# Kernel optimization log

Hardware: AMD Instinct MI355X
Metric: run time of the kernel (lower is better)

## Reference

```python
import jax, jax.numpy as jnp
import numpy as np
import math

DEPTH = 3
RATIO = 0.5
EPS = 1e-5


def _mlp_ln(h, W1, b1, W2, b2, W3, b3, g, beta):
    h = jax.nn.gelu(h @ W1 + b1, approximate=False)
    h = jax.nn.gelu(h @ W2 + b2, approximate=False)
    h = h @ W3 + b3
    mu = jnp.mean(h, axis=-1, keepdims=True)
    var = jnp.mean((h - mu) ** 2, axis=-1, keepdims=True)
    return g * (h - mu) * jax.lax.rsqrt(var + EPS) + beta


def _node_to_node(x, s, r, n, p):
    # two-way gather -> scatter_add -> MLP+LN. Row n of x_pad is a zero dummy
    # node that absorbs edges dropped by pooling (fixed-size, jit-friendly).
    x_pad = jnp.concatenate([x, jnp.zeros((1, x.shape[1]), x.dtype)], axis=0)
    msg = x_pad[jnp.concatenate([s, r])]            # [2E, C]
    recv = jnp.concatenate([r, s])                  # [2E]
    agg = jax.ops.segment_sum(msg, recv, num_segments=n + 1)[:n]
    return _mlp_ln(agg, *p)


def _forward(x, senders, receivers, pool_w, down_p, up_p):
    s, r = senders, receivers
    xs, edges, perms = [x], [(s, r)], []
    n = x.shape[0]
    for i in range(DEPTH):
        k = math.ceil(RATIO * n)  # PyG topk: ceil(ratio * N)
        w = pool_w[i]
        score = jnp.tanh(x @ w / jnp.linalg.norm(w))
        vals, perm = jax.lax.top_k(score, k)
        x = x[perm] * vals[:, None]
        # remap edges; dropped nodes (and old dummy n) map to new dummy k
        nmap = jnp.full((n + 1,), k, dtype=s.dtype).at[perm].set(
            jnp.arange(k, dtype=s.dtype))
        ns_, nr_ = nmap[s], nmap[r]
        invalid = (ns_ == k) | (nr_ == k)
        s = jnp.where(invalid, k, ns_)
        r = jnp.where(invalid, k, nr_)
        x = _node_to_node(x, s, r, k, down_p[i])
        if i < DEPTH - 1:
            xs.append(x)
            edges.append((s, r))
        perms.append(perm)
        n = k
    for i in range(DEPTH):
        j = DEPTH - 1 - i
        res = xs[j]
        s, r = edges[j]
        perm = perms[j]
        up = jnp.zeros_like(res).at[perm].set(x)
        x = jnp.concatenate([res, up], axis=-1)  # sum_res=False -> concat
        x = _node_to_node(x, s, r, res.shape[0], up_p[i])
    return x


def setup_inputs() -> dict:
    key = jax.random.key(0)
    ks = jax.random.split(key, 16)
    N, E, C, D = 50000, 600000, 128, DEPTH
    f32 = jnp.float32

    def lin(k, fi, fo):
        return (jax.random.normal(k, (D, fi, fo), f32) / np.sqrt(fi)).astype(f32)

    return {
        'x': jax.random.normal(ks[0], (N, C), f32),
        'senders': jax.random.randint(ks[1], (E,), 0, N, dtype=jnp.int32),
        'receivers': jax.random.randint(ks[2], (E,), 0, N, dtype=jnp.int32),
        'pool_w': jax.random.normal(ks[3], (D, C), f32),
        'down_W1': lin(ks[4], C, C), 'down_b1': jnp.zeros((D, C), f32),
        'down_W2': lin(ks[5], C, C), 'down_b2': jnp.zeros((D, C), f32),
        'down_W3': lin(ks[6], C, C), 'down_b3': jnp.zeros((D, C), f32),
        'down_g': jnp.ones((D, C), f32), 'down_beta': jnp.zeros((D, C), f32),
        'up_W1': lin(ks[7], 2 * C, C), 'up_b1': jnp.zeros((D, C), f32),
        'up_W2': lin(ks[8], C, C), 'up_b2': jnp.zeros((D, C), f32),
        'up_W3': lin(ks[9], C, C), 'up_b3': jnp.zeros((D, C), f32),
        'up_g': jnp.ones((D, C), f32), 'up_beta': jnp.zeros((D, C), f32),
    }


def reference(x, senders, receivers, pool_w,
              down_W1, down_b1, down_W2, down_b2, down_W3, down_b3,
              down_g, down_beta,
              up_W1, up_b1, up_W2, up_b2, up_W3, up_b3, up_g, up_beta):
    down_p = [(down_W1[i], down_b1[i], down_W2[i], down_b2[i],
               down_W3[i], down_b3[i], down_g[i], down_beta[i])
              for i in range(DEPTH)]
    up_p = [(up_W1[i], up_b1[i], up_W2[i], up_b2[i],
             up_W3[i], up_b3[i], up_g[i], up_beta[i])
            for i in range(DEPTH)]
    return _forward(x, senders, receivers, pool_w, down_p, up_p)
```

## Files before the change

kernel.cpp:

```cpp
#include <hip/hip_runtime.h>
#include <math.h>


typedef unsigned short u16;
typedef short bf16x8 __attribute__((ext_vector_type(8)));
typedef float f32x4 __attribute__((ext_vector_type(4)));

#define HIST_STRIDE (2 * 65536 + 512)
#define NB 128
#define NB_LOG 7
#define SUBR 5000

__device__ __forceinline__ unsigned int fkey(float f) {
  unsigned int b = __float_as_uint(f);
  return (b & 0x80000000u) ? ~b : (b | 0x80000000u);
}

__device__ __forceinline__ float gelu_f(float v) {
  return 0.5f * v * (1.0f + erff(v * 0.70710678118654752f));
}

__device__ __forceinline__ u16 f2bf(float f) {
  unsigned u = __float_as_uint(f);
  u = (u + 0x7FFFu + ((u >> 16) & 1u)) >> 16;
  return (u16)u;
}
__device__ __forceinline__ float bf2f(u16 u) {
  return __uint_as_float(((unsigned)u) << 16);
}

__global__ void score_kernel(const float* __restrict__ x, const float* __restrict__ w,
                             float* __restrict__ key, float* __restrict__ valt, int n) {
  int wave = threadIdx.x >> 6, lane = threadIdx.x & 63;
  int i = blockIdx.x * 4 + wave;
  if (i >= n) return;
  float2 xv = *(const float2*)&x[(size_t)i * 128 + lane * 2];
  float2 wv = *(const float2*)&w[lane * 2];
  double d  = (double)xv.x * wv.x + (double)xv.y * wv.y;
  double nw = (double)wv.x * wv.x + (double)wv.y * wv.y;
  for (int o = 32; o; o >>= 1) { d += __shfl_down(d, o, 64); nw += __shfl_down(nw, o, 64); }
  if (lane == 0) {
    key[i]  = (float)d;
    valt[i] = (float)tanh(d / sqrt(nw));
  }
}

__global__ void preamble_kernel(const float* __restrict__ x, u16* __restrict__ xb, int n,
                                const float* __restrict__ uW1, const float* __restrict__ uW2,
                                const float* __restrict__ uW3, u16* __restrict__ wt1,
                                u16* __restrict__ wt2, u16* __restrict__ wt3,
                                const float* __restrict__ poolw, double* __restrict__ sqn,
                                u16* __restrict__ z0, u16* __restrict__ z1,
                                u16* __restrict__ z2, int* __restrict__ histAll,
                                int nbX, int nbHZ, int nHist) {
  int b = blockIdx.x;
  if (b < nbX) {
    int gid = b * 256 + threadIdx.x;
    if (gid < n * 32) {
      float4 a = *(const float4*)&x[(size_t)gid * 4];
      *(ushort4*)&xb[(size_t)gid * 4] =
          make_ushort4(f2bf(a.x), f2bf(a.y), f2bf(a.z), f2bf(a.w));
    }
    return;
  }
  b -= nbX;
  if (b < 768) {
    int i = b * 256 + threadIdx.x;
    int lvl = i >> 16, rem = i & 65535;
    if (rem < 32768) {
      int k = rem >> 7, c = rem & 127;
      wt1[(size_t)lvl * 32768 + c * 256 + k] = f2bf(uW1[(size_t)lvl * 32768 + rem]);
    } else if (rem < 49152) {
      int j = rem - 32768; int k = j >> 7, c = j & 127;
      wt2[(size_t)lvl * 16384 + c * 128 + k] = f2bf(uW2[(size_t)lvl * 16384 + j]);
    } else {
      int j = rem - 49152; int k = j >> 7, c = j & 127;
      wt3[(size_t)lvl * 16384 + c * 128 + k] = f2bf(uW3[(size_t)lvl * 16384 + j]);
    }
    return;
  }
  b -= 768;
  if (b == 0) {
    if (threadIdx.x < 64) {
      int lane = threadIdx.x;
      for (int l = 0; l < 3; ++l) {
        float2 wv = *(const float2*)&poolw[l * 128 + lane * 2];
        double nw = (double)wv.x * wv.x + (double)wv.y * wv.y;
        for (int o = 32; o; o >>= 1) nw += __shfl_down(nw, o, 64);
        if (lane == 0) sqn[l] = sqrt(nw);
      }
    }
    return;
  }
  b -= 1;
  if (b == 0) {
    int t = threadIdx.x;
    if (t < 128) { z0[t] = 0; z1[t] = 0; z2[t] = 0; }
    return;
  }
  b -= 1;
  {
    int i = b * 256 + threadIdx.x;
    if (i < nHist) histAll[i] = 0;
  }
}

__global__ void hist_hi_kernel(const float* __restrict__ key, int* __restrict__ hist,
                               int* __restrict__ csum, int n) {
  __shared__ int lc[256];
  lc[threadIdx.x] = 0;
  __syncthreads();
  int i = blockIdx.x * 256 + threadIdx.x;
  if (i < n) {
    unsigned b = fkey(key[i]) >> 16;
    atomicAdd(&hist[b], 1);
    atomicAdd(&lc[b >> 8], 1);
  }
  __syncthreads();
  int v = lc[threadIdx.x];
  if (v) atomicAdd(&csum[threadIdx.x], v);
}

__global__ void hist_lo_kernel(const float* __restrict__ key, const int* __restrict__ meta,
                               int* __restrict__ hist, int* __restrict__ csum, int n) {
  __shared__ int lc[256];
  lc[threadIdx.x] = 0;
  __syncthreads();
  int i = blockIdx.x * 256 + threadIdx.x;
  if (i < n) {
    unsigned u = fkey(key[i]);
    if ((u >> 16) == (unsigned)meta[0]) {
      unsigned b = u & 0xFFFFu;
      atomicAdd(&hist[b], 1);
      atomicAdd(&lc[b >> 8], 1);
    }
  }
  __syncthreads();
  int v = lc[threadIdx.x];
  if (v) atomicAdd(&csum[threadIdx.x], v);
}

__device__ __forceinline__ void suffix_scan256(int* sA, int t) {
  for (int o = 1; o < 256; o <<= 1) {
    int add = (t + o < 256) ? sA[t + o] : 0;
    __syncthreads();
    sA[t] += add;
    __syncthreads();
  }
}

__global__ void find_hi2_kernel(const int* __restrict__ hist, const int* __restrict__ csum,
                                int* __restrict__ meta, int k) {
  __shared__ int sA[256];
  __shared__ int cSh, cumSh;
  int t = threadIdx.x;
  sA[t] = csum[t];
  __syncthreads();
  suffix_scan256(sA, t);
  int nxt = (t == 255) ? 0 : sA[t + 1];
  if (sA[t] >= k && nxt < k) { cSh = t; cumSh = nxt; }
  __syncthreads();
  int c = cSh;
  int k2 = k - cumSh;
  sA[t] = hist[c * 256 + t];
  __syncthreads();
  suffix_scan256(sA, t);
  nxt = (t == 255) ? 0 : sA[t + 1];
  if (sA[t] >= k2 && nxt < k2) {
    meta[0] = c * 256 + t;
    meta[1] = k2 - nxt;
  }
}

__global__ void find_lo2_kernel(const int* __restrict__ hist, const int* __restrict__ csum,
                                int* __restrict__ meta) {
  __shared__ int sA[256];
  __shared__ int cSh, cumSh;
  int t = threadIdx.x;
  int m = meta[1], B = meta[0];
  sA[t] = csum[t];
  __syncthreads();
  suffix_scan256(sA, t);
  int nxt = (t == 255) ? 0 : sA[t + 1];
  if (sA[t] >= m && nxt < m) { cSh = t; cumSh = nxt; }
  __syncthreads();
  int c = cSh;
  int m2 = m - cumSh;
  sA[t] = hist[c * 256 + t];
  __syncthreads();
  suffix_scan256(sA, t);
  nxt = (t == 255) ? 0 : sA[t + 1];
  if (sA[t] >= m2 && nxt < m2) {
    meta[3] = (int)((((unsigned)B) << 16) | (unsigned)(c * 256 + t));
    meta[4] = m2 - nxt;
  }
  if (t == 0) meta[5] = 0;
}

__global__ void tie_count_kernel(const float* __restrict__ key, const int* __restrict__ meta,
                                 int* __restrict__ tcnt, int n) {
  __shared__ int cnt[4];
  unsigned uT = (unsigned)meta[3];
  int i = blockIdx.x * 256 + threadIdx.x;
  bool tie = (i < n) && (fkey(key[i]) == uT);
  unsigned long long m = __ballot(tie);
  int lane = threadIdx.x & 63, w = threadIdx.x >> 6;
  if (lane == 0) cnt[w] = __popcll(m);
  __syncthreads();
  if (threadIdx.x == 0) tcnt[blockIdx.x] = cnt[0] + cnt[1] + cnt[2] + cnt[3];
}

__global__ void tie_select_kernel(const float* __restrict__ key, const float* __restrict__ valt,
                                  const int* __restrict__ tcnt, int* __restrict__ meta,
                                  int* __restrict__ perm, float* __restrict__ vals,
                                  int* __restrict__ nmap, int n, int k) {
  __shared__ int red[256];
  __shared__ int woff[4];
  int t = threadIdx.x;
  red[t] = (t < (int)blockIdx.x) ? tcnt[t] : 0;
  __syncthreads();
  for (int s = 128; s; s >>= 1) {
    if (t < s) red[t] += red[t + s];
    __syncthreads();
  }
  int blockbase = red[0];
  unsigned uT = (unsigned)meta[3];
  int tsel = meta[4];
  int i = blockIdx.x * 256 + t;
  unsigned u = (i < n) ? fkey(key[i]) : 0u;
  bool tie = (i < n) && (u == uT);
  unsigned long long m = __ballot(tie);
  int lane = t & 63, w = t >> 6;
  if (lane == 0) woff[w] = __popcll(m);
  __syncthreads();
  if (t == 0) {
    int c = 0;
    for (int q = 0; q < 4; ++q) { int v = woff[q]; woff[q] = c; c += v; }
  }
  __syncthreads();
  if (i > n) return;
  if (i == n) { nmap[n] = k; return; }
  bool sel;
  if (tie) {
    int pre = __popcll(m & ((1ull << lane) - 1ull));
    int rank = blockbase + woff[w] + pre;
    sel = (rank < tsel);
  } else {
    sel = (u > uT);
  }
  if (sel) {
    int slot = atomicAdd(&meta[5], 1);
    perm[slot] = i; vals[slot] = valt[i]; nmap[i] = slot;
  } else {
    nmap[i] = k;
  }
}

__global__ void pool_kernel(const float* __restrict__ x, const int* __restrict__ perm,
                            const float* __restrict__ vals, float* __restrict__ xp, int k) {
  int gid = blockIdx.x * 256 + threadIdx.x;
  int t = gid >> 5;
  if (t >= k) return;
  int c = (gid & 31) << 2;
  float v = vals[t];
  float4 a = *(const float4*)&x[(size_t)perm[t] * 128 + c];
  a.x *= v; a.y *= v; a.z *= v; a.w *= v;
  *(float4*)&xp[(size_t)t * 128 + c] = a;
}

__global__ void csr_count_kernel(const int* __restrict__ s, const int* __restrict__ r,
                                 int* __restrict__ H, int N, int E, int CH) {
  __shared__ int cnt[SUBR];
  int b = blockIdx.x & (NB - 1);
  int sub = blockIdx.x >> NB_LOG;
  int base = sub * SUBR;
  int top = base + SUBR; if (top > N) top = N;
  int span = top - base;
  for (int t = threadIdx.x; t < span; t += 256) cnt[t] = 0;
  __syncthreads();
  int lo = b * CH, hi = lo + CH; if (hi > E) hi = E;
  for (int e = lo + threadIdx.x; e < hi; e += 256) {
    int sv = s[e], rv = r[e];
    if ((unsigned)(rv - base) < (unsigned)span) atomicAdd(&cnt[rv - base], 1);
    if ((unsigned)(sv - base) < (unsigned)span) atomicAdd(&cnt[sv - base], 1);
  }
  __syncthreads();
  int* Hb = H + (size_t)b * N + base;
  for (int t = threadIdx.x; t < span; t += 256) Hb[t] = cnt[t];
}

__global__ void colsum_part_kernel(const int* __restrict__ H, int* __restrict__ deg,
                                   int* __restrict__ bsum, int n) {
  __shared__ int l[256];
  int i = blockIdx.x * 256 + threadIdx.x;
  int v = 0;
  if (i < n) {
#pragma unroll 4
    for (int b = 0; b < NB; ++b) v += H[(size_t)b * n + i];
    deg[i] = v;
  }
  l[threadIdx.x] = (i < n) ? v : 0;
  __syncthreads();
  for (int s = 128; s; s >>= 1) {
    if (threadIdx.x < s) l[threadIdx.x] += l[threadIdx.x + s];
    __syncthreads();
  }
  if (threadIdx.x == 0) bsum[blockIdx.x] = l[0];
}

__global__ void scanfix_kernel(const int* __restrict__ deg, const int* __restrict__ bsum,
                               int* __restrict__ off, int* __restrict__ H, int n) {
  __shared__ int red[256];
  __shared__ int l[256];
  int i = blockIdx.x * 256 + threadIdx.x;
  int t = threadIdx.x;
  red[t] = (t < (int)blockIdx.x) ? bsum[t] : 0;
  __syncthreads();
  for (int s = 128; s; s >>= 1) {
    if (t < s) red[t] += red[t + s];
    __syncthreads();
  }
  int base = red[0];
  int v = (i < n) ? deg[i] : 0;
  l[t] = v;
  __syncthreads();
#pragma unroll
  for (int s = 1; s < 256; s <<= 1) {
    int add = (t >= s) ? l[t - s] : 0;
    __syncthreads();
    l[t] += add;
    __syncthreads();
  }
  int incl = l[t];
  if (i < n) {
    int e = base + incl - v;
    off[i] = e;
    if (i == n - 1) off[n] = base + incl;
    int run = e;
#pragma unroll 4
    for (int b = 0; b < NB; ++b) {
      size_t id = (size_t)b * n + i;
      int tv = H[id];
      H[id] = run;
      run += tv;
    }
  }
}

__global__ void csr_scatter_lds_kernel(const int* __restrict__ s, const int* __restrict__ r,
                                       const int* __restrict__ H, int* __restrict__ idx,
                                       int N, int E, int CH) {
  __shared__ int cnt[SUBR];
  int b = blockIdx.x & (NB - 1);
  int sub = blockIdx.x >> NB_LOG;
  int base = sub * SUBR;
  int top = base + SUBR; if (top > N) top = N;
  int span = top - base;
  for (int t = threadIdx.x; t < span; t += 256) cnt[t] = 0;
  __syncthreads();
  int lo = b * CH, hi = lo + CH; if (hi > E) hi = E;
  const int* Hb = H + (size_t)b * N;
  for (int e = lo + threadIdx.x; e < hi; e += 256) {
    int sv = s[e], rv = r[e];
    if ((unsigned)(rv - base) < (unsigned)span) {
      int loc = atomicAdd(&cnt[rv - base], 1);
      idx[Hb[rv] + loc] = sv;
    }
    if ((unsigned)(sv - base) < (unsigned)span) {
      int loc = atomicAdd(&cnt[sv - base], 1);
      idx[Hb[sv] + loc] = rv;
    }
  }
}

__global__ void derive_deg_kernel(const int* __restrict__ permL, const int* __restrict__ nm,
                                  const int* __restrict__ offP, const int* __restrict__ idxP,
                                  int* __restrict__ deg, int k) {
  int wave = threadIdx.x >> 6, lane = threadIdx.x & 63;
  int v = blockIdx.x * 4 + wave;
  if (v >= k) return;
  int p = permL[v];
  int lo = __builtin_amdgcn_readfirstlane(offP[p]);
  int hi = __builtin_amdgcn_readfirstlane(offP[p + 1]);
  int cnt = 0;
  for (int j0 = lo; j0 < hi; j0 += 64) {
    int j = j0 + lane;
    bool ok = (j < hi) && (nm[idxP[j]] < k);
    unsigned long long msk = __ballot(ok);
    cnt += __popcll(msk);
  }
  if (lane == 0) deg[v] = cnt;
}

__global__ void derive_fill_kernel(const int* __restrict__ permL, const int* __restrict__ nm,
                                   const int* __restrict__ offP, const int* __restrict__ idxP,
                                   const int* __restrict__ offL, int* __restrict__ idxL,
                                   int k) {
  int wave = threadIdx.x >> 6, lane = threadIdx.x & 63;
  int v = blockIdx.x * 4 + wave;
  if (v >= k) return;
  int p = permL[v];
  int lo = __builtin_amdgcn_readfirstlane(offP[p]);
  int hi = __builtin_amdgcn_readfirstlane(offP[p + 1]);
  int base = __builtin_amdgcn_readfirstlane(offL[v]);
  for (int j0 = lo; j0 < hi; j0 += 64) {
    int j = j0 + lane;
    int m = k;
    if (j < hi) m = nm[idxP[j]];
    bool ok = m < k;
    unsigned long long msk = __ballot(ok);
    int rank = __popcll(msk & ((1ull << lane) - 1ull));
    if (ok) idxL[base + rank] = m;
    base += __popcll(msk);
  }
}

__global__ void scan_part_kernel(const int* __restrict__ deg, int* __restrict__ bsum, int n) {
  __shared__ int l[256];
  int i = blockIdx.x * 256 + threadIdx.x;
  l[threadIdx.x] = (i < n) ? deg[i] : 0;
  __syncthreads();
  for (int s = 128; s; s >>= 1) {
    if (threadIdx.x < s) l[threadIdx.x] += l[threadIdx.x + s];
    __syncthreads();
  }
  if (threadIdx.x == 0) bsum[blockIdx.x] = l[0];
}

__global__ void scan_final_kernel(const int* __restrict__ deg, const int* __restrict__ bsum,
                                  int* __restrict__ off, int n) {
  __shared__ int red[256];
  __shared__ int l[256];
  int i = blockIdx.x * 256 + threadIdx.x;
  int t = threadIdx.x;
  red[t] = (t < (int)blockIdx.x) ? bsum[t] : 0;
  __syncthreads();
  for (int s = 128; s; s >>= 1) {
    if (t < s) red[t] += red[t + s];
    __syncthreads();
  }
  int base = red[0];
  int v = (i < n) ? deg[i] : 0;
  l[t] = v;
  __syncthreads();
#pragma unroll
  for (int s = 1; s < 256; s <<= 1) {
    int add = (t >= s) ? l[t - s] : 0;
    __syncthreads();
    l[t] += add;
    __syncthreads();
  }
  int incl = l[t];
  if (i < n) {
    int e = base + incl - v;
    off[i] = e;
    if (i == n - 1) off[n] = base + incl;
  }
}

__global__ void idxup3_kernel(const int* __restrict__ idxA, const int* __restrict__ nmA,
                              const int* __restrict__ lenA, int* __restrict__ outA,
                              const int* __restrict__ idxB, const int* __restrict__ nmB,
                              const int* __restrict__ lenB, int* __restrict__ outB,
                              const int* __restrict__ idxC, const int* __restrict__ nmC,
                              const int* __restrict__ lenC, int* __restrict__ outC,
                              int nbSeg, int maxlen) {
  int seg = blockIdx.x / nbSeg;
  int j = (blockIdx.x - seg * nbSeg) * 256 + threadIdx.x;
  if (j >= maxlen) return;
  const int* idx; const int* nm; const int* len; int* out;
  if (seg == 0)      { idx = idxA; nm = nmA; len = lenA; out = outA; }
  else if (seg == 1) { idx = idxB; nm = nmB; len = lenB; out = outB; }
  else               { idx = idxC; nm = nmC; len = lenC; out = outC; }
  if (j >= len[0]) return;
  out[j] = nm[idx[j]];
}

__global__ void agg_kernel(const float* __restrict__ x, const int* __restrict__ off,
                           const int* __restrict__ idx, float* __restrict__ agg, int n) {
  int wave = threadIdx.x >> 6, lane = threadIdx.x & 63;
  int v = blockIdx.x * 4 + wave;
  if (v >= n) return;
  int lo = __builtin_amdgcn_readfirstlane(off[v]);
  int hi = __builtin_amdgcn_readfirstlane(off[v + 1]);
  int g = lane >> 5, sl = lane & 31;
  const float* bp = x + sl * 4;
  float4 acc = {0.f, 0.f, 0.f, 0.f};
#define ACC_F(EE)                                        \
  do {                                                   \
    float4 w_ = *(const float4*)(bp + (size_t)(EE) * 128);\
    acc.x += w_.x; acc.y += w_.y; acc.z += w_.z; acc.w += w_.w; \
  } while (0)
  int j = lo;
  for (; j + 8 <= hi; j += 8) {
    int q0 = idx[j],     q1 = idx[j + 1], q2 = idx[j + 2], q3 = idx[j + 3];
    int q4 = idx[j + 4], q5 = idx[j + 5], q6 = idx[j + 6], q7 = idx[j + 7];
    ACC_F(g ? q1 : q0);
    ACC_F(g ? q3 : q2);
    ACC_F(g ? q5 : q4);
    ACC_F(g ? q7 : q6);
  }
  for (; j + 2 <= hi; j += 2) {
    int q0 = idx[j], q1 = idx[j + 1];
    ACC_F(g ? q1 : q0);
  }
  if (j < hi) {
    int q0 = idx[j];
    if (!g) ACC_F(q0);
  }
#undef ACC_F
  acc.x += __shfl_xor(acc.x, 32, 64);
  acc.y += __shfl_xor(acc.y, 32, 64);
  acc.z += __shfl_xor(acc.z, 32, 64);
  acc.w += __shfl_xor(acc.w, 32, 64);
  if (!g) *(float4*)&agg[(size_t)v * 128 + sl * 4] = acc;
}

__global__ void agg_gather2_kernel(const u16* __restrict__ tabR, const int* __restrict__ idxR,
                                   const u16* __restrict__ tabU, const int* __restrict__ idxU,
                                   const int* __restrict__ off, u16* __restrict__ agg,
                                   int n, int nbHalf) {
  bool upH = (int)blockIdx.x >= nbHalf;
  int blk = upH ? (int)blockIdx.x - nbHalf : (int)blockIdx.x;
  const u16* tab = upH ? tabU : tabR;
  const int* idx = upH ? idxU : idxR;
  int OFS = upH ? 128 : 0;
  int wave = threadIdx.x >> 6, lane = threadIdx.x & 63;
  int v = blk * 4 + wave;
  if (v >= n) return;
  int lo = __builtin_amdgcn_readfirstlane(off[v]);
  int hi = __builtin_amdgcn_readfirstlane(off[v + 1]);
  int g = lane >> 4, sl = lane & 15;
  const u16* bp = tab + sl * 8;
  float4 a0 = {0.f, 0.f, 0.f, 0.f}, a1 = {0.f, 0.f, 0.f, 0.f};

#define ACC_ROW(EE)                                     \
  do {                                                  \
    uint4 wq = *(const uint4*)(bp + (size_t)(EE) * 128);\
    a0.x += __uint_as_float(wq.x << 16);                \
    a0.y += __uint_as_float(wq.x & 0xffff0000u);        \
    a0.z += __uint_as_float(wq.y << 16);                \
    a0.w += __uint_as_float(wq.y & 0xffff0000u);        \
    a1.x += __uint_as_float(wq.z << 16);                \
    a1.y += __uint_as_float(wq.z & 0xffff0000u);        \
    a1.z += __uint_as_float(wq.w << 16);                \
    a1.w += __uint_as_float(wq.w & 0xffff0000u);        \
  } while (0)

  int j = lo;
  for (; j + 16 <= hi; j += 16) {
    int e0 = idx[j + g];
    int e1 = idx[j + g + 4];
    int e2 = idx[j + g + 8];
    int e3 = idx[j + g + 12];
    ACC_ROW(e0); ACC_ROW(e1); ACC_ROW(e2); ACC_ROW(e3);
  }
  for (; j + 4 <= hi; j += 4) {
    int e0 = idx[j + g];
    ACC_ROW(e0);
  }
  int rmn = hi - j;
  if (g < rmn) {
    int e = idx[j + g];
    ACC_ROW(e);
  }
#undef ACC_ROW

  a0.x += __shfl_xor(a0.x, 16, 64);
  a0.y += __shfl_xor(a0.y, 16, 64);
  a0.z += __shfl_xor(a0.z, 16, 64);
  a0.w += __shfl_xor(a0.w, 16, 64);
  a1.x += __shfl_xor(a1.x, 16, 64);
  a1.y += __shfl_xor(a1.y, 16, 64);
  a1.z += __shfl_xor(a1.z, 16, 64);
  a1.w += __shfl_xor(a1.w, 16, 64);
  a0.x += __shfl_xor(a0.x, 32, 64);
  a0.y += __shfl_xor(a0.y, 32, 64);
  a0.z += __shfl_xor(a0.z, 32, 64);
  a0.w += __shfl_xor(a0.w, 32, 64);
  a1.x += __shfl_xor(a1.x, 32, 64);
  a1.y += __shfl_xor(a1.y, 32, 64);
  a1.z += __shfl_xor(a1.z, 32, 64);
  a1.w += __shfl_xor(a1.w, 32, 64);

  if (lane < 16) {
    bf16x8 ov;
    ov[0] = (short)f2bf(a0.x); ov[1] = (short)f2bf(a0.y);
    ov[2] = (short)f2bf(a0.z); ov[3] = (short)f2bf(a0.w);
    ov[4] = (short)f2bf(a1.x); ov[5] = (short)f2bf(a1.y);
    ov[6] = (short)f2bf(a1.z); ov[7] = (short)f2bf(a1.w);
    *(bf16x8*)&agg[(size_t)v * 256 + OFS + sl * 8] = ov;
  }
}

template <bool SCORE>
__global__ __launch_bounds__(256) void mlp_down_kernel(
    const float* __restrict__ A,
    const float* __restrict__ W1, const float* __restrict__ b1,
    const float* __restrict__ W2, const float* __restrict__ b2,
    const float* __restrict__ W3, const float* __restrict__ b3,
    const float* __restrict__ g, const float* __restrict__ beta,
    float* __restrict__ out, u16* __restrict__ outbf,
    const float* __restrict__ wnext, const double* __restrict__ sqn,
    float* __restrict__ key, float* __restrict__ valt, int n) {
  __shared__ float cur[32 * 128];
  __shared__ float As[32 * 32];
  __shared__ float Ws[32 * 128];
  int t = threadIdx.x;
  int row0 = blockIdx.x * 32;
  int colg = (t & 31) << 2;
  int rowg = (t >> 5) << 2;
  float acc[4][4];
  const float* Wl[3] = {W1, W2, W3};
  const float* bl[3] = {b1, b2, b3};
#pragma unroll
  for (int l = 0; l < 3; ++l) {
    const float* W = Wl[l];
#pragma unroll
    for (int i = 0; i < 4; ++i)
#pragma unroll
      for (int j = 0; j < 4; ++j) acc[i][j] = 0.f;
    for (int k0 = 0; k0 < 128; k0 += 32) {
      __syncthreads();
      {
        int ar = t >> 3, ac = (t & 7) << 2;
        float4 av;
        if (l == 0) {
          av = make_float4(0.f, 0.f, 0.f, 0.f);
          if (row0 + ar < n) av = *(const float4*)&A[(size_t)(row0 + ar) * 128 + k0 + ac];
        } else {
          av = *(const float4*)&cur[ar * 128 + k0 + ac];
        }
        *(float4*)&As[ar * 32 + ac] = av;
      }
#pragma unroll
      for (int ll = 0; ll < 4; ++ll) {
        int id = t + ll * 256;
        int kk = id >> 5, wc = (id & 31) << 2;
        *(float4*)&Ws[kk * 128 + wc] = *(const float4*)&W[(size_t)(k0 + kk) * 128 + wc];
      }
      __syncthreads();
#pragma unroll
      for (int kk = 0; kk < 32; kk += 4) {
        float4 wv[4];
#pragma unroll
        for (int j = 0; j < 4; ++j) wv[j] = *(const float4*)&Ws[(kk + j) * 128 + colg];
#pragma unroll
        for (int i = 0; i < 4; ++i) {
          float4 av = *(const float4*)&As[(rowg + i) * 32 + kk];
          acc[i][0] += av.x * wv[0].x + av.y * wv[1].x + av.z * wv[2].x + av.w * wv[3].x;
          acc[i][1] += av.x * wv[0].y + av.y * wv[1].y + av.z * wv[2].y + av.w * wv[3].y;
          acc[i][2] += av.x * wv[0].z + av.y * wv[1].z + av.z * wv[2].z + av.w * wv[3].z;
          acc[i][3] += av.x * wv[0].w + av.y * wv[1].w + av.z * wv[2].w + av.w * wv[3].w;
        }
      }
    }
    float4 bv = *(const float4*)&bl[l][colg];
    if (l < 2) {
      __syncthreads();
#pragma unroll
      for (int i = 0; i < 4; ++i) {
        float4 o = make_float4(gelu_f(acc[i][0] + bv.x), gelu_f(acc[i][1] + bv.y),
                               gelu_f(acc[i][2] + bv.z), gelu_f(acc[i][3] + bv.w));
        *(float4*)&cur[(rowg + i) * 128 + colg] = o;
      }
    } else {
#pragma unroll
      for (int i = 0; i < 4; ++i) {
        acc[i][0] += bv.x; acc[i][1] += bv.y; acc[i][2] += bv.z; acc[i][3] += bv.w;
      }
    }
  }
  float4 gvv = *(const float4*)&g[colg];
  float4 bev = *(const float4*)&beta[colg];
  float4 wv4 = make_float4(0.f, 0.f, 0.f, 0.f);
  if (SCORE) wv4 = *(const float4*)&wnext[colg];
#pragma unroll
  for (int i = 0; i < 4; ++i) {
    float s1 = acc[i][0] + acc[i][1] + acc[i][2] + acc[i][3];
#pragma unroll
    for (int o = 1; o <= 16; o <<= 1) s1 += __shfl_xor(s1, o, 64);
    float mu = s1 * (1.0f / 128.0f);
    float d0 = acc[i][0] - mu, d1 = acc[i][1] - mu, d2 = acc[i][2] - mu, d3 = acc[i][3] - mu;
    float s2 = d0 * d0 + d1 * d1 + d2 * d2 + d3 * d3;
#pragma unroll
    for (int o = 1; o <= 16; o <<= 1) s2 += __shfl_xor(s2, o, 64);
    float rs = rsqrtf(s2 * (1.0f / 128.0f) + 1e-5f);
    int rr = row0 + rowg + i;
    float o0 = gvv.x * d0 * rs + bev.x;
    float o1 = gvv.y * d1 * rs + bev.y;
    float o2 = gvv.z * d2 * rs + bev.z;
    float o3 = gvv.w * d3 * rs + bev.w;
    if (rr < n) {
      *(float4*)&out[(size_t)rr * 128 + colg] = make_float4(o0, o1, o2, o3);
      *(ushort4*)&outbf[(size_t)rr * 128 + colg] =
          make_ushort4(f2bf(o0), f2bf(o1), f2bf(o2), f2bf(o3));
    }
    if (SCORE) {
      double d = (double)o0 * wv4.x + (double)o1 * wv4.y +
                 (double)o2 * wv4.z + (double)o3 * wv4.w;
#pragma unroll
      for (int o = 1; o <= 16; o <<= 1) d += __shfl_xor(d, o, 64);
      if ((t & 31) == 0 && rr < n) {
        key[rr]  = (float)d;
        valt[rr] = (float)tanh(d / sqn[0]);
      }
    }
  }
}

template <bool WF32, bool WBF>
__global__ __launch_bounds__(256) void mlp_up_kernel(
    const u16* __restrict__ A,
    const u16* __restrict__ WT1, const float* __restrict__ b1,
    const u16* __restrict__ WT2, const float* __restrict__ b2,
    const u16* __restrict__ WT3, const float* __restrict__ b3,
    const float* __restrict__ g, const float* __restrict__ beta,
    float* __restrict__ out, u16* __restrict__ outbf, int n) {
  __shared__ u16 As[64 * 72];
  __shared__ u16 Ws[128 * 72];
  __shared__ u16 cur[64 * 136];
  int t = threadIdx.x;
  int lane = t & 63, wave = t >> 6;
  int row0 = blockIdx.x * 64;
  int colb = lane & 15, rquad = lane >> 4;
  f32x4 acc[8];

#pragma unroll
  for (int i = 0; i < 8; ++i) acc[i] = (f32x4){0.f, 0.f, 0.f, 0.f};
  for (int k0 = 0; k0 < 256; k0 += 64) {
    __syncthreads();
#pragma unroll
    for (int i = 0; i < 2; ++i) {
      int c = t + i * 256;
      int r = c >> 3, seg = c & 7;
      bf16x8 v = {0, 0, 0, 0, 0, 0, 0, 0};
      if (row0 + r < n) v = *(const bf16x8*)&A[(size_t)(row0 + r) * 256 + k0 + seg * 8];
      *(bf16x8*)&As[r * 72 + seg * 8] = v;
    }
#pragma unroll
    for (int i = 0; i < 4; ++i) {
      int c = t + i * 256;
      int r = c >> 3, seg = c & 7;
      *(bf16x8*)&Ws[r * 72 + seg * 8] = *(const bf16x8*)&WT1[(size_t)r * 256 + k0 + seg * 8];
    }
    __syncthreads();
#pragma unroll
    for (int kk = 0; kk < 64; kk += 32) {
      bf16x8 a = *(const bf16x8*)&As[(wave * 16 + (lane & 15)) * 72 + kk + (lane >> 4) * 8];
#pragma unroll
      for (int ct = 0; ct < 8; ++ct) {
        bf16x8 b = *(const bf16x8*)&Ws[(ct * 16 + (lane & 15)) * 72 + kk + (lane >> 4) * 8];
        acc[ct] = __builtin_amdgcn_mfma_f32_16x16x32_bf16(a, b, acc[ct], 0, 0, 0);
      }
    }
  }
  __syncthreads();
#pragma unroll
  for (int ct = 0; ct < 8; ++ct) {
    int col = ct * 16 + colb;
    float bb = b1[col];
#pragma unroll
    for (int r = 0; r < 4; ++r) {
      int row = wave * 16 + rquad * 4 + r;
      cur[row * 136 + col] = f2bf(gelu_f(acc[ct][r] + bb));
    }
  }

#pragma unroll
  for (int i = 0; i < 8; ++i) acc[i] = (f32x4){0.f, 0.f, 0.f, 0.f};
  for (int k0 = 0; k0 < 128; k0 += 64) {
    __syncthreads();
#pragma unroll
    for (int i = 0; i < 4; ++i) {
      int c = t + i * 256;
      int r = c >> 3, seg = c & 7;
      *(bf16x8*)&Ws[r * 72 + seg * 8] = *(const bf16x8*)&WT2[(size_t)r * 128 + k0 + seg * 8];
    }
    __syncthreads();
#pragma unroll
    for (int kk = 0; kk < 64; kk += 32) {
      bf16x8 a = *(const bf16x8*)&cur[(wave * 16 + (lane & 15)) * 136 + k0 + kk + (lane >> 4) * 8];
#pragma unroll
      for (int ct = 0; ct < 8; ++ct) {
        bf16x8 b = *(const bf16x8*)&Ws[(ct * 16 + (lane & 15)) * 72 + kk + (lane >> 4) * 8];
        acc[ct] = __builtin_amdgcn_mfma_f32_16x16x32_bf16(a, b, acc[ct], 0, 0, 0);
      }
    }
  }
  __syncthreads();
#pragma unroll
  for (int ct = 0; ct < 8; ++ct) {
    int col = ct * 16 + colb;
    float bb = b2[col];
#pragma unroll
    for (int r = 0; r < 4; ++r) {
      int row = wave * 16 + rquad * 4 + r;
      cur[row * 136 + col] = f2bf(gelu_f(acc[ct][r] + bb));
    }
  }

#pragma unroll
  for (int i = 0; i < 8; ++i) acc[i] = (f32x4){0.f, 0.f, 0.f, 0.f};
  for (int k0 = 0; k0 < 128; k0 += 64) {
    __syncthreads();
#pragma unroll
    for (int i = 0; i < 4; ++i) {
      int c = t + i * 256;
      int r = c >> 3, seg = c & 7;
      *(bf16x8*)&Ws[r * 72 + seg * 8] = *(const bf16x8*)&WT3[(size_t)r * 128 + k0 + seg * 8];
    }
    __syncthreads();
#pragma unroll
    for (int kk = 0; kk < 64; kk += 32) {
      bf16x8 a = *(const bf16x8*)&cur[(wave * 16 + (lane & 15)) * 136 + k0 + kk + (lane >> 4) * 8];
#pragma unroll
      for (int ct = 0; ct < 8; ++ct) {
        bf16x8 b = *(const bf16x8*)&Ws[(ct * 16 + (lane & 15)) * 72 + kk + (lane >> 4) * 8];
        acc[ct] = __builtin_amdgcn_mfma_f32_16x16x32_bf16(a, b, acc[ct], 0, 0, 0);
      }
    }
  }
  float bv[8], gv[8], bev[8];
#pragma unroll
  for (int ct = 0; ct < 8; ++ct) {
    int col = ct * 16 + colb;
    bv[ct] = b3[col]; gv[ct] = g[col]; bev[ct] = beta[col];
  }
#pragma unroll
  for (int r = 0; r < 4; ++r) {
    float s1 = 0.f;
#pragma unroll
    for (int ct = 0; ct < 8; ++ct) s1 += acc[ct][r] + bv[ct];
#pragma unroll
    for (int o = 1; o <= 8; o <<= 1) s1 += __shfl_xor(s1, o, 64);
    float mu = s1 * (1.0f / 128.0f);
    float s2 = 0.f;
#pragma unroll
    for (int ct = 0; ct < 8; ++ct) { float d = acc[ct][r] + bv[ct] - mu; s2 += d * d; }
#pragma unroll
    for (int o = 1; o <= 8; o <<= 1) s2 += __shfl_xor(s2, o, 64);
    float rs = rsqrtf(s2 * (1.0f / 128.0f) + 1e-5f);
    int row = row0 + wave * 16 + rquad * 4 + r;
    if (row < n) {
#pragma unroll
      for (int ct = 0; ct < 8; ++ct) {
        int col = ct * 16 + colb;
        float o = gv[ct] * (acc[ct][r] + bv[ct] - mu) * rs + bev[ct];
        if (WF32) out[(size_t)row * 128 + col] = o;
        if (WBF)  outbf[(size_t)row * 128 + col] = f2bf(o);
      }
    }
  }
}


static inline int cdiv(int a, int b) { return (a + b - 1) / b; }

extern "C" void kernel_launch(void* const* d_in, const int* in_sizes, int n_in,
                              void* d_out, int out_size, void* d_ws, size_t ws_size,
                              hipStream_t stream) {
  const float* x0   = (const float*)d_in[0];
  const int*   snd  = (const int*)d_in[1];
  const int*   rcv  = (const int*)d_in[2];
  const float* poolw = (const float*)d_in[3];
  const float* dW1 = (const float*)d_in[4];
  const float* db1 = (const float*)d_in[5];
  const float* dW2 = (const float*)d_in[6];
  const float* db2 = (const float*)d_in[7];
  const float* dW3 = (const float*)d_in[8];
  const float* db3 = (const float*)d_in[9];
  const float* dg  = (const float*)d_in[10];
  const float* dbe = (const float*)d_in[11];
  const float* uW1 = (const float*)d_in[12];
  const float* ub1 = (const float*)d_in[13];
  const float* uW2 = (const float*)d_in[14];
  const float* ub2 = (const float*)d_in[15];
  const float* uW3 = (const float*)d_in[16];
  const float* ub3 = (const float*)d_in[17];
  const float* ug  = (const float*)d_in[18];
  const float* ube = (const float*)d_in[19];

  const int N0 = in_sizes[0] / 128;
  const int E  = in_sizes[1];
  const int N1 = (N0 + 1) / 2, N2 = (N1 + 1) / 2, N3 = (N2 + 1) / 2;

  char* p = (char*)d_ws;
  auto alloc = [&](size_t bytes) -> void* {
    void* r = (void*)p;
    p += (bytes + 255) & ~(size_t)255;
    return r;
  };
  float* key  = (float*)alloc((size_t)N0 * 4);
  float* valt = (float*)alloc((size_t)N0 * 4);
  int*   histAll = (int*)alloc((size_t)3 * HIST_STRIDE * 4);
  int*   meta = (int*)alloc(64 * 4);
  int*   tcnt = (int*)alloc(512 * 4);
  int*   bsum = (int*)alloc(256 * 4);
  int*   nm1 = (int*)alloc((size_t)(N0 + 1) * 4);
  int*   nm2 = (int*)alloc((size_t)(N1 + 1) * 4);
  int*   nm3 = (int*)alloc((size_t)(N2 + 1) * 4);
  int*   perm0 = (int*)alloc((size_t)N1 * 4);
  int*   perm1 = (int*)alloc((size_t)N2 * 4);
  int*   perm2 = (int*)alloc((size_t)N3 * 4);
  float* vals  = (float*)alloc((size_t)N1 * 4);
  double* sqn  = (double*)alloc(8 * 8);
  float* x1 = (float*)alloc((size_t)N1 * 128 * 4);
  float* x2 = (float*)alloc((size_t)N2 * 128 * 4);
  float* x3 = (float*)alloc((size_t)N3 * 128 * 4);
  float* xp = (float*)alloc((size_t)N1 * 128 * 4);
  float* aggf = (float*)alloc((size_t)N1 * 128 * 4);
  u16* agg_bf = (u16*)alloc((size_t)N0 * 256 * 2);
  u16* res0_bf = (u16*)alloc((size_t)N0 * 128 * 2);
  u16* res1_bf = (u16*)alloc((size_t)N1 * 128 * 2);
  u16* res2_bf = (u16*)alloc((size_t)N2 * 128 * 2);
  u16* x3_bf   = (u16*)alloc((size_t)(N3 + 1) * 128 * 2);
  u16* xu2_bf  = (u16*)alloc((size_t)(N2 + 1) * 128 * 2);
  u16* xu1_bf  = (u16*)alloc((size_t)(N1 + 1) * 128 * 2);
  u16* wt1 = (u16*)alloc((size_t)3 * 128 * 256 * 2);
  u16* wt2 = (u16*)alloc((size_t)3 * 128 * 128 * 2);
  u16* wt3 = (u16*)alloc((size_t)3 * 128 * 128 * 2);
  int* degAll = (int*)alloc((size_t)(N0 + N1 + N2 + N3) * 4);
  int* deg0 = degAll;
  int* deg1 = degAll + N0;
  int* deg2 = deg1 + N1;
  int* deg3 = deg2 + N2;
  int* off0 = (int*)alloc((size_t)(N0 + 1) * 4);
  int* idx0 = (int*)alloc((size_t)2 * E * 4);
  int* off1 = (int*)alloc((size_t)(N1 + 1) * 4);
  int* idx1 = (int*)alloc((size_t)2 * E * 4);
  int* off2 = (int*)alloc((size_t)(N2 + 1) * 4);
  int* idx2 = (int*)alloc((size_t)2 * E * 4);
  int* off3 = (int*)alloc((size_t)(N3 + 1) * 4);
  int* idx3 = (int*)alloc((size_t)2 * E * 4);
  int* idxu0 = (int*)alloc((size_t)2 * E * 4);
  int* idxu1 = (int*)alloc((size_t)2 * E * 4);
  int* idxu2 = (int*)alloc((size_t)2 * E * 4);
  int* H = (int*)alloc((size_t)NB * N0 * 4);

  {
    int nbX = cdiv(N0 * 32, 256);
    int nHist = 3 * HIST_STRIDE;
    int nbHZ = cdiv(nHist, 256);
    preamble_kernel<<<nbX + 768 + 1 + 1 + nbHZ, 256, 0, stream>>>(
        x0, res0_bf, N0, uW1, uW2, uW3, wt1, wt2, wt3, poolw, sqn,
        x3_bf + (size_t)N3 * 128, xu2_bf + (size_t)N2 * 128,
        xu1_bf + (size_t)N1 * 128, histAll, nbX, nbHZ, nHist);
  }

  {
    int nSub = cdiv(N0, SUBR);
    int CH = cdiv(E, NB);
    int nbN = cdiv(N0, 256);
    csr_count_kernel<<<NB * nSub, 256, 0, stream>>>(snd, rcv, H, N0, E, CH);
    colsum_part_kernel<<<nbN, 256, 0, stream>>>(H, deg0, bsum, N0);
    scanfix_kernel<<<nbN, 256, 0, stream>>>(deg0, bsum, off0, H, N0);
    csr_scatter_lds_kernel<<<NB * nSub, 256, 0, stream>>>(snd, rcv, H, idx0, N0, E, CH);
  }

  auto run_scan = [&](int* degB, int* offB, int n) {
    int nb = cdiv(n, 256);
    scan_part_kernel<<<nb, 256, 0, stream>>>(degB, bsum, n);
    scan_final_kernel<<<nb, 256, 0, stream>>>(degB, bsum, offB, n);
  };

  auto down_step = [&](int n, int k, const float* xcur, int* permL, int* nmL,
                       float* xnext, u16* xnext_bf, int lvl,
                       const int* offP, const int* idxP,
                       int* offL, int* degL, int* idxL) {
    int nb = cdiv(n, 256);
    int* histL = histAll + (size_t)lvl * HIST_STRIDE;
    int* csum_hi = histL + 2 * 65536;
    int* csum_lo = csum_hi + 256;
    hist_hi_kernel<<<nb, 256, 0, stream>>>(key, histL, csum_hi, n);
    find_hi2_kernel<<<1, 256, 0, stream>>>(histL, csum_hi, meta, k);
    hist_lo_kernel<<<nb, 256, 0, stream>>>(key, meta, histL + 65536, csum_lo, n);
    find_lo2_kernel<<<1, 256, 0, stream>>>(histL + 65536, csum_lo, meta);
    tie_count_kernel<<<nb, 256, 0, stream>>>(key, meta, tcnt, n);
    tie_select_kernel<<<cdiv(n + 1, 256), 256, 0, stream>>>(
        key, valt, tcnt, meta, permL, vals, nmL, n, k);
    pool_kernel<<<cdiv(k * 32, 256), 256, 0, stream>>>(xcur, permL, vals, xp, k);
    derive_deg_kernel<<<cdiv(k, 4), 256, 0, stream>>>(permL, nmL, offP, idxP, degL, k);
    run_scan(degL, offL, k);
    derive_fill_kernel<<<cdiv(k, 4), 256, 0, stream>>>(permL, nmL, offP, idxP, offL, idxL, k);
    agg_kernel<<<cdiv(k, 4), 256, 0, stream>>>(xp, offL, idxL, aggf, k);
    if (lvl < 2)
      mlp_down_kernel<true><<<cdiv(k, 32), 256, 0, stream>>>(
          aggf,
          dW1 + (size_t)lvl * 128 * 128, db1 + (size_t)lvl * 128,
          dW2 + (size_t)lvl * 128 * 128, db2 + (size_t)lvl * 128,
          dW3 + (size_t)lvl * 128 * 128, db3 + (size_t)lvl * 128,
          dg + (size_t)lvl * 128, dbe + (size_t)lvl * 128,
          xnext, xnext_bf, poolw + (size_t)(lvl + 1) * 128, sqn + (lvl + 1),
          key, valt, k);
    else
      mlp_down_kernel<false><<<cdiv(k, 32), 256, 0, stream>>>(
          aggf,
          dW1 + (size_t)lvl * 128 * 128, db1 + (size_t)lvl * 128,
          dW2 + (size_t)lvl * 128 * 128, db2 + (size_t)lvl * 128,
          dW3 + (size_t)lvl * 128 * 128, db3 + (size_t)lvl * 128,
          dg + (size_t)lvl * 128, dbe + (size_t)lvl * 128,
          xnext, xnext_bf, nullptr, nullptr, nullptr, nullptr, k);
  };

  score_kernel<<<cdiv(N0, 4), 256, 0, stream>>>(x0, poolw, key, valt, N0);
  down_step(N0, N1, x0, perm0, nm1, x1, res1_bf, 0, off0, idx0, off1, deg1, idx1);
  down_step(N1, N2, x1, perm1, nm2, x2, res2_bf, 1, off1, idx1, off2, deg2, idx2);
  down_step(N2, N3, x2, perm2, nm3, x3, x3_bf,   2, off2, idx2, off3, deg3, idx3);

  {
    int nbSeg = cdiv(2 * E, 256);
    idxup3_kernel<<<3 * nbSeg, 256, 0, stream>>>(
        idx2, nm3, off2 + N2, idxu2,
        idx1, nm2, off1 + N1, idxu1,
        idx0, nm1, off0 + N0, idxu0, nbSeg, 2 * E);
  }

  auto up_step = [&](int n, const u16* resb, const u16* xdb, int lvl,
                     const int* offL, const int* idxL, const int* idxUL,
                     bool wantF32, float* outF32, u16* outBF) {
    int nbh = cdiv(n, 4);
    agg_gather2_kernel<<<2 * nbh, 256, 0, stream>>>(
        resb, idxL, xdb, idxUL, offL, agg_bf, n, nbh);
    if (wantF32)
      mlp_up_kernel<true, false><<<cdiv(n, 64), 256, 0, stream>>>(
          agg_bf,
          wt1 + (size_t)lvl * 128 * 256, ub1 + (size_t)lvl * 128,
          wt2 + (size_t)lvl * 128 * 128, ub2 + (size_t)lvl * 128,
          wt3 + (size_t)lvl * 128 * 128, ub3 + (size_t)lvl * 128,
          ug + (size_t)lvl * 128, ube + (size_t)lvl * 128,
          outF32, nullptr, n);
    else
      mlp_up_kernel<false, true><<<cdiv(n, 64), 256, 0, stream>>>(
          agg_bf,
          wt1 + (size_t)lvl * 128 * 256, ub1 + (size_t)lvl * 128,
          wt2 + (size_t)lvl * 128 * 128, ub2 + (size_t)lvl * 128,
          wt3 + (size_t)lvl * 128 * 128, ub3 + (size_t)lvl * 128,
          ug + (size_t)lvl * 128, ube + (size_t)lvl * 128,
          nullptr, outBF, n);
  };

  up_step(N2, res2_bf, x3_bf,  0, off2, idx2, idxu2, false, nullptr, xu2_bf);
  up_step(N1, res1_bf, xu2_bf, 1, off1, idx1, idxu1, false, nullptr, xu1_bf);
  up_step(N0, res0_bf, xu1_bf, 2, off0, idx0, idxu0, true, (float*)d_out, nullptr);

  (void)n_in; (void)out_size; (void)ws_size;
}
```

Measured before the change: 821.1 us.

## Merge pool and degree kernels, single-block scan, split down MLP into three GEMMs

Pooling and degree counting now run as one launch, with blocks dispatched by index range. The two-kernel block scan is replaced by a single-block serial scan over all k entries. The fused three-layer down MLP kernel is split into two GEMM+GELU kernels and a GEMM+LayerNorm kernel, which write intermediates to new global buffers. This removes launch overhead and LDS pressure per kernel, but adds global round trips for the intermediates and serialises the scan onto one block.

```diff
diff --git a/kernel.cpp b/kernel.cpp
--- a/kernel.cpp
+++ b/kernel.cpp
@@ -256,16 +256,38 @@
   }
 }
 
-__global__ void pool_kernel(const float* __restrict__ x, const int* __restrict__ perm,
-                            const float* __restrict__ vals, float* __restrict__ xp, int k) {
-  int gid = blockIdx.x * 256 + threadIdx.x;
-  int t = gid >> 5;
-  if (t >= k) return;
-  int c = (gid & 31) << 2;
-  float v = vals[t];
-  float4 a = *(const float4*)&x[(size_t)perm[t] * 128 + c];
-  a.x *= v; a.y *= v; a.z *= v; a.w *= v;
-  *(float4*)&xp[(size_t)t * 128 + c] = a;
+__global__ void pool_derive_kernel(const float* __restrict__ x, const int* __restrict__ perm,
+                                   const float* __restrict__ vals, float* __restrict__ xp,
+                                   const int* __restrict__ nm, const int* __restrict__ offP,
+                                   const int* __restrict__ idxP, int* __restrict__ deg,
+                                   int k, int nbPool) {
+  int b = blockIdx.x;
+  if (b < nbPool) {
+    int gid = b * 256 + threadIdx.x;
+    int tt = gid >> 5;
+    if (tt >= k) return;
+    int c = (gid & 31) << 2;
+    float v = vals[tt];
+    float4 a = *(const float4*)&x[(size_t)perm[tt] * 128 + c];
+    a.x *= v; a.y *= v; a.z *= v; a.w *= v;
+    *(float4*)&xp[(size_t)tt * 128 + c] = a;
+    return;
+  }
+  b -= nbPool;
+  int wave = threadIdx.x >> 6, lane = threadIdx.x & 63;
+  int v = b * 4 + wave;
+  if (v >= k) return;
+  int p = perm[v];
+  int lo = __builtin_amdgcn_readfirstlane(offP[p]);
+  int hi = __builtin_amdgcn_readfirstlane(offP[p + 1]);
+  int cnt = 0;
+  for (int j0 = lo; j0 < hi; j0 += 64) {
+    int j = j0 + lane;
+    bool ok = (j < hi) && (nm[idxP[j]] < k);
+    unsigned long long msk = __ballot(ok);
+    cnt += __popcll(msk);
+  }
+  if (lane == 0) deg[v] = cnt;
 }
 
 __global__ void csr_count_kernel(const int* __restrict__ s, const int* __restrict__ r,
@@ -371,25 +393,6 @@
       idx[Hb[sv] + loc] = rv;
     }
   }
-}
-
-__global__ void derive_deg_kernel(const int* __restrict__ permL, const int* __restrict__ nm,
-                                  const int* __restrict__ offP, const int* __restrict__ idxP,
-                                  int* __restrict__ deg, int k) {
-  int wave = threadIdx.x >> 6, lane = threadIdx.x & 63;
-  int v = blockIdx.x * 4 + wave;
-  if (v >= k) return;
-  int p = permL[v];
-  int lo = __builtin_amdgcn_readfirstlane(offP[p]);
-  int hi = __builtin_amdgcn_readfirstlane(offP[p + 1]);
-  int cnt = 0;
-  for (int j0 = lo; j0 < hi; j0 += 64) {
-    int j = j0 + lane;
-    bool ok = (j < hi) && (nm[idxP[j]] < k);
-    unsigned long long msk = __ballot(ok);
-    cnt += __popcll(msk);
-  }
-  if (lane == 0) deg[v] = cnt;
 }
 
 __global__ void derive_fill_kernel(const int* __restrict__ permL, const int* __restrict__ nm,
@@ -415,46 +418,31 @@
   }
 }
 
-__global__ void scan_part_kernel(const int* __restrict__ deg, int* __restrict__ bsum, int n) {
+__global__ void scan_single_kernel(const int* __restrict__ deg, int* __restrict__ off, int n) {
   __shared__ int l[256];
-  int i = blockIdx.x * 256 + threadIdx.x;
-  l[threadIdx.x] = (i < n) ? deg[i] : 0;
-  __syncthreads();
-  for (int s = 128; s; s >>= 1) {
-    if (threadIdx.x < s) l[threadIdx.x] += l[threadIdx.x + s];
-    __syncthreads();
-  }
-  if (threadIdx.x == 0) bsum[blockIdx.x] = l[0];
-}
-
-__global__ void scan_final_kernel(const int* __restrict__ deg, const int* __restrict__ bsum,
-                                  int* __restrict__ off, int n) {
-  __shared__ int red[256];
-  __shared__ int l[256];
-  int i = blockIdx.x * 256 + threadIdx.x;
+  __shared__ int runSh;
   int t = threadIdx.x;
-  red[t] = (t < (int)blockIdx.x) ? bsum[t] : 0;
-  __syncthreads();
-  for (int s = 128; s; s >>= 1) {
-    if (t < s) red[t] += red[t + s];
-    __syncthreads();
-  }
-  int base = red[0];
-  int v = (i < n) ? deg[i] : 0;
-  l[t] = v;
-  __syncthreads();
-#pragma unroll
-  for (int s = 1; s < 256; s <<= 1) {
-    int add = (t >= s) ? l[t - s] : 0;
-    __syncthreads();
-    l[t] += add;
-    __syncthreads();
-  }
-  int incl = l[t];
-  if (i < n) {
-    int e = base + incl - v;
-    off[i] = e;
-    if (i == n - 1) off[n] = base + incl;
+  if (t == 0) runSh = 0;
+  __syncthreads();
+  for (int base = 0; base < n; base += 256) {
+    int i = base + t;
+    int v = (i < n) ? deg[i] : 0;
+    l[t] = v;
+    __syncthreads();
+#pragma unroll
+    for (int s = 1; s < 256; s <<= 1) {
+      int add = (t >= s) ? l[t - s] : 0;
+      __syncthreads();
+      l[t] += add;
+      __syncthreads();
+    }
+    int incl = l[t];
+    int run = runSh;
+    if (i < n) off[i] = run + incl - v;
+    if (i == n - 1) off[n] = run + incl;
+    __syncthreads();
+    if (t == 255) runSh = run + l[255];
+    __syncthreads();
   }
 }
 
@@ -593,17 +581,11 @@
   }
 }
 
-template <bool SCORE>
-__global__ __launch_bounds__(256) void mlp_down_kernel(
-    const float* __restrict__ A,
-    const float* __restrict__ W1, const float* __restrict__ b1,
-    const float* __restrict__ W2, const float* __restrict__ b2,
-    const float* __restrict__ W3, const float* __restrict__ b3,
-    const float* __restrict__ g, const float* __restrict__ beta,
-    float* __restrict__ out, u16* __restrict__ outbf,
-    const float* __restrict__ wnext, const double* __restrict__ sqn,
-    float* __restrict__ key, float* __restrict__ valt, int n) {
-  __shared__ float cur[32 * 128];
+template <bool GELU>
+__global__ __launch_bounds__(256) void gemm_kernel(const float* __restrict__ A,
+                                                   const float* __restrict__ W,
+                                                   const float* __restrict__ bias,
+                                                   float* __restrict__ out, int n) {
   __shared__ float As[32 * 32];
   __shared__ float Ws[32 * 128];
   int t = threadIdx.x;
@@ -611,65 +593,107 @@
   int colg = (t & 31) << 2;
   int rowg = (t >> 5) << 2;
   float acc[4][4];
-  const float* Wl[3] = {W1, W2, W3};
-  const float* bl[3] = {b1, b2, b3};
-#pragma unroll
-  for (int l = 0; l < 3; ++l) {
-    const float* W = Wl[l];
-#pragma unroll
-    for (int i = 0; i < 4; ++i)
-#pragma unroll
-      for (int j = 0; j < 4; ++j) acc[i][j] = 0.f;
-    for (int k0 = 0; k0 < 128; k0 += 32) {
-      __syncthreads();
-      {
-        int ar = t >> 3, ac = (t & 7) << 2;
-        float4 av;
-        if (l == 0) {
-          av = make_float4(0.f, 0.f, 0.f, 0.f);
-          if (row0 + ar < n) av = *(const float4*)&A[(size_t)(row0 + ar) * 128 + k0 + ac];
-        } else {
-          av = *(const float4*)&cur[ar * 128 + k0 + ac];
-        }
-        *(float4*)&As[ar * 32 + ac] = av;
+#pragma unroll
+  for (int i = 0; i < 4; ++i)
+#pragma unroll
+    for (int j = 0; j < 4; ++j) acc[i][j] = 0.f;
+
+  for (int k0 = 0; k0 < 128; k0 += 32) {
+    __syncthreads();
+    {
+      int ar = t >> 3, ac = (t & 7) << 2;
+      float4 av = make_float4(0.f, 0.f, 0.f, 0.f);
+      if (row0 + ar < n) av = *(const float4*)&A[(size_t)(row0 + ar) * 128 + k0 + ac];
+      *(float4*)&As[ar * 32 + ac] = av;
+    }
+#pragma unroll
+    for (int l = 0; l < 4; ++l) {
+      int id = t + l * 256;
+      int kk = id >> 5, wc = (id & 31) << 2;
+      *(float4*)&Ws[kk * 128 + wc] = *(const float4*)&W[(size_t)(k0 + kk) * 128 + wc];
+    }
+    __syncthreads();
+#pragma unroll
+    for (int kk = 0; kk < 32; kk += 4) {
+      float4 wv[4];
+#pragma unroll
+      for (int j = 0; j < 4; ++j) wv[j] = *(const float4*)&Ws[(kk + j) * 128 + colg];
+#pragma unroll
+      for (int i = 0; i < 4; ++i) {
+        float4 av = *(const float4*)&As[(rowg + i) * 32 + kk];
+        acc[i][0] += av.x * wv[0].x + av.y * wv[1].x + av.z * wv[2].x + av.w * wv[3].x;
+        acc[i][1] += av.x * wv[0].y + av.y * wv[1].y + av.z * wv[2].y + av.w * wv[3].y;
+        acc[i][2] += av.x * wv[0].z + av.y * wv[1].z + av.z * wv[2].z + av.w * wv[3].z;
+        acc[i][3] += av.x * wv[0].w + av.y * wv[1].w + av.z * wv[2].w + av.w * wv[3].w;
       }
-#pragma unroll
-      for (int ll = 0; ll < 4; ++ll) {
-        int id = t + ll * 256;
-        int kk = id >> 5, wc = (id & 31) << 2;
-        *(float4*)&Ws[kk * 128 + wc] = *(const float4*)&W[(size_t)(k0 + kk) * 128 + wc];
+    }
+  }
+  float4 bv = *(const float4*)&bias[colg];
+#pragma unroll
+  for (int i = 0; i < 4; ++i) {
+    int rr = row0 + rowg + i;
+    if (rr < n) {
+      float4 o = make_float4(acc[i][0] + bv.x, acc[i][1] + bv.y, acc[i][2] + bv.z, acc[i][3] + bv.w);
+      if (GELU) { o.x = gelu_f(o.x); o.y = gelu_f(o.y); o.z = gelu_f(o.z); o.w = gelu_f(o.w); }
+      *(float4*)&out[(size_t)rr * 128 + colg] = o;
+    }
+  }
+}
+
+template <bool SCORE>
+__global__ __launch_bounds__(256) void gemm_ln_kernel(
+    const float* __restrict__ A, const float* __restrict__ W,
+    const float* __restrict__ bias, const float* __restrict__ g,
+    const float* __restrict__ beta, float* __restrict__ out,
+    u16* __restrict__ outbf, const float* __restrict__ wnext,
+    const double* __restrict__ sqn, float* __restrict__ key,
+    float* __restrict__ valt, int n) {
+  __shared__ float As[32 * 32];
+  __shared__ float Ws[32 * 128];
+  int t = threadIdx.x;
+  int row0 = blockIdx.x * 32;
+  int colg = (t & 31) << 2;
+  int rowg = (t >> 5) << 2;
+  float acc[4][4];
+#pragma unroll
+  for (int i = 0; i < 4; ++i)
+#pragma unroll
+    for (int j = 0; j < 4; ++j) acc[i][j] = 0.f;
+
+  for (int k0 = 0; k0 < 128; k0 += 32) {
+    __syncthreads();
+    {
+      int ar = t >> 3, ac = (t & 7) << 2;
+      float4 av = make_float4(0.f, 0.f, 0.f, 0.f);
+      if (row0 + ar < n) av = *(const float4*)&A[(size_t)(row0 + ar) * 128 + k0 + ac];
+      *(float4*)&As[ar * 32 + ac] = av;
+    }
+#pragma unroll
+    for (int l = 0; l < 4; ++l) {
+      int id = t + l * 256;
+      int kk = id >> 5, wc = (id & 31) << 2;
+      *(float4*)&Ws[kk * 128 + wc] = *(const float4*)&W[(size_t)(k0 + kk) * 128 + wc];
+    }
+    __syncthreads();
+#pragma unroll
+    for (int kk = 0; kk < 32; kk += 4) {
+      float4 wv[4];
+#pragma unroll
+      for (int j = 0; j < 4; ++j) wv[j] = *(const float4*)&Ws[(kk + j) * 128 + colg];
+#pragma unroll
+      for (int i = 0; i < 4; ++i) {
+        float4 av = *(const float4*)&As[(rowg + i) * 32 + kk];
+        acc[i][0] += av.x * wv[0].x + av.y * wv[1].x + av.z * wv[2].x + av.w * wv[3].x;
+        acc[i][1] += av.x * wv[0].y + av.y * wv[1].y + av.z * wv[2].y + av.w * wv[3].y;
+        acc[i][2] += av.x * wv[0].z + av.y * wv[1].z + av.z * wv[2].z + av.w * wv[3].z;
+        acc[i][3] += av.x * wv[0].w + av.y * wv[1].w + av.z * wv[2].w + av.w * wv[3].w;
       }
-      __syncthreads();
-#pragma unroll
-      for (int kk = 0; kk < 32; kk += 4) {
-        float4 wv[4];
-#pragma unroll
-        for (int j = 0; j < 4; ++j) wv[j] = *(const float4*)&Ws[(kk + j) * 128 + colg];
-#pragma unroll
-        for (int i = 0; i < 4; ++i) {
-          float4 av = *(const float4*)&As[(rowg + i) * 32 + kk];
-          acc[i][0] += av.x * wv[0].x + av.y * wv[1].x + av.z * wv[2].x + av.w * wv[3].x;
-          acc[i][1] += av.x * wv[0].y + av.y * wv[1].y + av.z * wv[2].y + av.w * wv[3].y;
-          acc[i][2] += av.x * wv[0].z + av.y * wv[1].z + av.z * wv[2].z + av.w * wv[3].z;
-          acc[i][3] += av.x * wv[0].w + av.y * wv[1].w + av.z * wv[2].w + av.w * wv[3].w;
-        }
-      }
-    }
-    float4 bv = *(const float4*)&bl[l][colg];
-    if (l < 2) {
-      __syncthreads();
-#pragma unroll
-      for (int i = 0; i < 4; ++i) {
-        float4 o = make_float4(gelu_f(acc[i][0] + bv.x), gelu_f(acc[i][1] + bv.y),
-                               gelu_f(acc[i][2] + bv.z), gelu_f(acc[i][3] + bv.w));
-        *(float4*)&cur[(rowg + i) * 128 + colg] = o;
-      }
-    } else {
-#pragma unroll
-      for (int i = 0; i < 4; ++i) {
-        acc[i][0] += bv.x; acc[i][1] += bv.y; acc[i][2] += bv.z; acc[i][3] += bv.w;
-      }
-    }
+    }
+  }
+  float4 bv = *(const float4*)&bias[colg];
+#pragma unroll
+  for (int i = 0; i < 4; ++i) {
+    acc[i][0] += bv.x; acc[i][1] += bv.y; acc[i][2] += bv.z; acc[i][3] += bv.w;
   }
   float4 gvv = *(const float4*)&g[colg];
   float4 bev = *(const float4*)&beta[colg];
@@ -910,6 +934,8 @@
   float* x3 = (float*)alloc((size_t)N3 * 128 * 4);
   float* xp = (float*)alloc((size_t)N1 * 128 * 4);
   float* aggf = (float*)alloc((size_t)N1 * 128 * 4);
+  float* h1f  = (float*)alloc((size_t)N1 * 128 * 4);
+  float* h2f  = (float*)alloc((size_t)N1 * 128 * 4);
   u16* agg_bf = (u16*)alloc((size_t)N0 * 256 * 2);
   u16* res0_bf = (u16*)alloc((size_t)N0 * 128 * 2);
   u16* res1_bf = (u16*)alloc((size_t)N1 * 128 * 2);
@@ -958,12 +984,6 @@
     csr_scatter_lds_kernel<<<NB * nSub, 256, 0, stream>>>(snd, rcv, H, idx0, N0, E, CH);
   }
 
-  auto run_scan = [&](int* degB, int* offB, int n) {
-    int nb = cdiv(n, 256);
-    scan_part_kernel<<<nb, 256, 0, stream>>>(degB, bsum, n);
-    scan_final_kernel<<<nb, 256, 0, stream>>>(degB, bsum, offB, n);
-  };
-
   auto down_step = [&](int n, int k, const float* xcur, int* permL, int* nmL,
                        float* xnext, u16* xnext_bf, int lvl,
                        const int* offP, const int* idxP,
@@ -979,28 +999,29 @@
     tie_count_kernel<<<nb, 256, 0, stream>>>(key, meta, tcnt, n);
     tie_select_kernel<<<cdiv(n + 1, 256), 256, 0, stream>>>(
         key, valt, tcnt, meta, permL, vals, nmL, n, k);
-    pool_kernel<<<cdiv(k * 32, 256), 256, 0, stream>>>(xcur, permL, vals, xp, k);
-    derive_deg_kernel<<<cdiv(k, 4), 256, 0, stream>>>(permL, nmL, offP, idxP, degL, k);
-    run_scan(degL, offL, k);
+    {
+      int nbPool = cdiv(k * 32, 256);
+      int nbDeg = cdiv(k, 4);
+      pool_derive_kernel<<<nbPool + nbDeg, 256, 0, stream>>>(
+          xcur, permL, vals, xp, nmL, offP, idxP, degL, k, nbPool);
+    }
+    scan_single_kernel<<<1, 256, 0, stream>>>(degL, offL, k);
     derive_fill_kernel<<<cdiv(k, 4), 256, 0, stream>>>(permL, nmL, offP, idxP, offL, idxL, k);
     agg_kernel<<<cdiv(k, 4), 256, 0, stream>>>(xp, offL, idxL, aggf, k);
+    gemm_kernel<true><<<cdiv(k, 32), 256, 0, stream>>>(
+        aggf, dW1 + (size_t)lvl * 128 * 128, db1 + (size_t)lvl * 128, h1f, k);
+    gemm_kernel<true><<<cdiv(k, 32), 256, 0, stream>>>(
+        h1f, dW2 + (size_t)lvl * 128 * 128, db2 + (size_t)lvl * 128, h2f, k);
     if (lvl < 2)
-      mlp_down_kernel<true><<<cdiv(k, 32), 256, 0, stream>>>(
-          aggf,
-          dW1 + (size_t)lvl * 128 * 128, db1 + (size_t)lvl * 128,
-          dW2 + (size_t)lvl * 128 * 128, db2 + (size_t)lvl * 128,
-          dW3 + (size_t)lvl * 128 * 128, db3 + (size_t)lvl * 128,
-          dg + (size_t)lvl * 128, dbe + (size_t)lvl * 128,
-          xnext, xnext_bf, poolw + (size_t)(lvl + 1) * 128, sqn + (lvl + 1),
-          key, valt, k);
+      gemm_ln_kernel<true><<<cdiv(k, 32), 256, 0, stream>>>(
+          h2f, dW3 + (size_t)lvl * 128 * 128, db3 + (size_t)lvl * 128,
+          dg + (size_t)lvl * 128, dbe + (size_t)lvl * 128, xnext, xnext_bf,
+          poolw + (size_t)(lvl + 1) * 128, sqn + (lvl + 1), key, valt, k);
     else
-      mlp_down_kernel<false><<<cdiv(k, 32), 256, 0, stream>>>(
-          aggf,
-          dW1 + (size_t)lvl * 128 * 128, db1 + (size_t)lvl * 128,
-          dW2 + (size_t)lvl * 128 * 128, db2 + (size_t)lvl * 128,
-          dW3 + (size_t)lvl * 128 * 128, db3 + (size_t)lvl * 128,
-          dg + (size_t)lvl * 128, dbe + (size_t)lvl * 128,
-          xnext, xnext_bf, nullptr, nullptr, nullptr, nullptr, k);
+      gemm_ln_kernel<false><<<cdiv(k, 32), 256, 0, stream>>>(
+          h2f, dW3 + (size_t)lvl * 128 * 128, db3 + (size_t)lvl * 128,
+          dg + (size_t)lvl * 128, dbe + (size_t)lvl * 128, xnext, xnext_bf,
+          nullptr, nullptr, nullptr, nullptr, k);
   };
 
   score_kernel<<<cdiv(N0, 4), 256, 0, stream>>>(x0, poolw, key, valt, N0);
```

After: 941.8 us. +14.7%, slower.
